# Kernel optimization log

Measured on AMD Instinct MI355X. Metric: run time of the kernel, lower is better.

The kernel has to match this reference:

```python
import jax, jax.numpy as jnp
import numpy as np

B = 131072
IN, H1, H2, OUT = 784, 128, 64, 10


def setup_inputs() -> dict:
    key = jax.random.key(0)
    ks = jax.random.split(key, 10)
    f16 = jnp.float16
    x = jax.random.normal(ks[0], (B, IN), dtype=f16)
    # int4 quantized weights: values in [-8, 7], stored as int32
    w1_q = jax.random.randint(ks[1], (H1, IN), -8, 8, dtype=jnp.int32)
    w2_q = jax.random.randint(ks[2], (H2, H1), -8, 8, dtype=jnp.int32)
    w3_q = jax.random.randint(ks[3], (OUT, H2), -8, 8, dtype=jnp.int32)
    # per-output-channel scales ~ kaiming-ish magnitude / 7 (int4 max)
    s1 = (jax.random.uniform(ks[4], (H1,), dtype=f16) * f16(0.02) + f16(0.005))
    s2 = (jax.random.uniform(ks[5], (H2,), dtype=f16) * f16(0.02) + f16(0.005))
    s3 = (jax.random.uniform(ks[6], (OUT,), dtype=f16) * f16(0.02) + f16(0.005))
    b1 = jax.random.normal(ks[7], (H1,), dtype=f16) * f16(0.01)
    b2 = jax.random.normal(ks[8], (H2,), dtype=f16) * f16(0.01)
    b3 = jax.random.normal(ks[9], (OUT,), dtype=f16) * f16(0.01)
    return {"x": x, "w1_q": w1_q, "s1": s1, "b1": b1,
            "w2_q": w2_q, "s2": s2, "b2": b2,
            "w3_q": w3_q, "s3": s3, "b3": b3}


def _qlinear(x, w_q, scale, bias):
    # W4A16: dequantize int4 weights with per-out-channel scale, fp16 GEMM + bias
    w = w_q.astype(jnp.float16) * scale[:, None]  # [out, in]
    return jnp.dot(x, w.T) + bias


def reference(x, w1_q, s1, b1, w2_q, s2, b2, w3_q, s3, b3):
    x = x.reshape(-1, IN)
    h = jax.nn.relu(_qlinear(x, w1_q, s1, b1))
    h = jax.nn.relu(_qlinear(h, w2_q, s2, b2))
    return _qlinear(h, w3_q, s3, b3)
```

## Files before the change

### kernel.cpp

```cpp
#include <hip/hip_runtime.h>
#include <hip/hip_bf16.h>

#define NROWS 131072
#define KIN   784
#define H1N   128
#define H2N   64
#define OUTN  10

#define W1P_DWORDS (25 * 4 * 128)
#define W2C_ELEMS  (16 * 64 * 8)
#define W3_ELEMS   (16 * 64)

typedef short s16x8 __attribute__((ext_vector_type(8)));
typedef float f32x4 __attribute__((ext_vector_type(4)));

typedef __hip_bfloat16 bf16;

static __device__ __forceinline__ short b2s(float f) {
    bf16 h = __float2bfloat16(f);
    return *reinterpret_cast<short*>(&h);
}

static __device__ __forceinline__ s16x8 cvt8(f32x4 a, f32x4 b) {
    s16x8 r;
    r[0] = b2s(a[0]); r[1] = b2s(a[1]); r[2] = b2s(a[2]); r[3] = b2s(a[3]);
    r[4] = b2s(b[0]); r[5] = b2s(b[1]); r[6] = b2s(b[2]); r[7] = b2s(b[3]);
    return r;
}

static __device__ __forceinline__ s16x8 unpack8(unsigned d) {
    s16x8 r;
#pragma unroll
    for (int j = 0; j < 8; ++j) {
        int v = ((int)(d << (28 - 4 * j))) >> 28;
        r[j] = b2s((float)v);
    }
    return r;
}

static __device__ __forceinline__ void gl2lds16(const void* g, char* l) {
    __builtin_amdgcn_global_load_lds(
        (const __attribute__((address_space(1))) void*)g,
        (__attribute__((address_space(3))) void*)l, 16, 0, 0);
}
static __device__ __forceinline__ void gl2lds4(const void* g, char* l) {
    __builtin_amdgcn_global_load_lds(
        (const __attribute__((address_space(1))) void*)g,
        (__attribute__((address_space(3))) void*)l, 4, 0, 0);
}

#define WAITV(N) do { asm volatile("s_waitcnt vmcnt(" #N ")" ::: "memory"); \
                      __builtin_amdgcn_sched_barrier(0); } while (0)
#define WAITL()  do { asm volatile("s_waitcnt lgkmcnt(0)" ::: "memory"); \
                      __builtin_amdgcn_sched_barrier(0); } while (0)
#define BAR()    __builtin_amdgcn_s_barrier()

__global__ __launch_bounds__(256) void dequant_kernel(
    const int* __restrict__ w1q, const float* __restrict__ s1,
    const int* __restrict__ w2q, const float* __restrict__ s2,
    const int* __restrict__ w3q, const float* __restrict__ s3,
    unsigned* __restrict__ w1p, bf16* __restrict__ w2c, bf16* __restrict__ w3d)
{
    const int total = W1P_DWORDS + W2C_ELEMS + W3_ELEMS;
    for (int i = blockIdx.x * blockDim.x + threadIdx.x; i < total;
         i += gridDim.x * blockDim.x) {
        if (i < W1P_DWORDS) {
            int kb = i >> 9, rem = i & 511;
            int kg = rem >> 7, col_s = rem & 127;
            int col = (col_s - 8 * kg) & 127;
            unsigned d = 0;
#pragma unroll
            for (int j = 0; j < 8; ++j) {
                int k = kb * 32 + kg * 8 + j;
                unsigned q = 0;
                if (k < KIN) q = (unsigned)w1q[col * KIN + k] & 0xFu;
                d |= q << (4 * j);
            }
            w1p[i] = d;
        } else if (i < W1P_DWORDS + W2C_ELEMS) {
            int t = i - W1P_DWORDS;
            int kb = t >> 9, rem = t & 511;
            int col = rem >> 3, j = rem & 7;
            int k = kb * 8 + j;
            w2c[t] = __float2bfloat16((float)w2q[col * H1N + k] * s2[col]);
        } else {
            int t = i - W1P_DWORDS - W2C_ELEMS;
            int r = t >> 6, c = t & 63;
            float v = 0.0f;
            if (r < OUTN) v = (float)w3q[r * H2N + c] * s3[r];
            w3d[t] = __float2bfloat16(v);
        }
    }
}

__global__ __launch_bounds__(256, 6) void mlp_kernel(
    const float* __restrict__ x,
    const unsigned* __restrict__ w1p,
    const bf16*  __restrict__ w2c,
    const bf16*  __restrict__ w3d,
    const float* __restrict__ s1,
    const float* __restrict__ b1,
    const float* __restrict__ b2,
    const float* __restrict__ b3,
    float* __restrict__ out)
{
    __shared__ __align__(16) char lds[20480];

    const int tid  = threadIdx.x;
    const int lane = tid & 63;
    const int wv   = tid >> 6;
    const int r16  = lane & 15;
    const int kg   = lane >> 4;
    const int kgo  = kg * 8;

    const int i3 = lane >> 3;
    const int i7 = lane & 7;
    const int sw = i7 ^ i3;
    const int adj = (sw >= 4) ? 16 : 0;

    const long long rowW = (long long)blockIdx.x * 64 + wv * 16;
    const float* gA = x + (rowW + i3) * (long long)KIN + sw * 4;
    const unsigned* gB = w1p + wv * 128 + lane;

    const int aoff0 = wv * 2048 + r16 * 128 + (((2 * kg) ^ (r16 & 7)) * 16);

#pragma unroll
    for (int w = 0; w < 2; ++w) {
        char* ad = lds + w * 8192 + wv * 2048;
        gl2lds16(gA + w * 32, ad);
        gl2lds16(gA + w * 32 + 8 * KIN, ad + 1024);
        char* bd = lds + 16384 + w * 2048 + wv * 512;
        const unsigned* gb = gB + w * 512;
        gl2lds4(gb, bd);
        gl2lds4(gb + 64, bd + 256);
    }

    f32x4 acc1[8];
#pragma unroll
    for (int j = 0; j < 8; ++j) acc1[j] = (f32x4){0.f, 0.f, 0.f, 0.f};

#pragma unroll 1
    for (int t = 0; t < 24; ++t) {
        WAITV(4);
        BAR();
        const char* sa = lds + (t & 1) * 8192;
        f32x4 q0 = *(const f32x4*)(sa + aoff0);
        f32x4 q1 = *(const f32x4*)(sa + (aoff0 ^ 16));
        const char* sbB = lds + 16384 + (t & 1) * 2048 + kg * 512;
        unsigned bd[8];
#pragma unroll
        for (int nj = 0; nj < 8; ++nj)
            bd[nj] = *(const unsigned*)(sbB + (((nj * 16 + r16 + 8 * kg) & 127) << 2));
        WAITL();
        BAR();
        if (t < 22) {
            char* ad = lds + (t & 1) * 8192 + wv * 2048;
            const float* g = gA + (t + 2) * 32;
            gl2lds16(g, ad);
            gl2lds16(g + 8 * KIN, ad + 1024);
            char* bdst = lds + 16384 + (t & 1) * 2048 + wv * 512;
            const unsigned* gb = gB + (t + 2) * 512;
            gl2lds4(gb, bdst);
            gl2lds4(gb + 64, bdst + 256);
        } else if (t == 22) {
            char* ad = lds + (t & 1) * 8192 + wv * 2048;
            const float* g = gA + 768 - adj;
            gl2lds16(g, ad);
            gl2lds16(g + 8 * KIN, ad + 1024);
            char* bdst = lds + 16384 + (t & 1) * 2048 + wv * 512;
            const unsigned* gb = gB + 24 * 512;
            gl2lds4(gb, bdst);
            gl2lds4(gb + 64, bdst + 256);
        }
        s16x8 a = cvt8(q0, q1);
#pragma unroll
        for (int nj = 0; nj < 8; ++nj) {
            s16x8 bf = unpack8(bd[nj]);
            acc1[nj] = __builtin_amdgcn_mfma_f32_16x16x32_bf16(a, bf, acc1[nj], 0, 0, 0);
        }
    }
    {
        WAITV(0);
        BAR();
        const char* sa = lds;
        f32x4 q0 = *(const f32x4*)(sa + aoff0);
        f32x4 q1 = *(const f32x4*)(sa + (aoff0 ^ 16));
        const char* sbB = lds + 16384 + kg * 512;
        unsigned bd[8];
#pragma unroll
        for (int nj = 0; nj < 8; ++nj)
            bd[nj] = *(const unsigned*)(sbB + (((nj * 16 + r16 + 8 * kg) & 127) << 2));
        WAITL();
        BAR();
        s16x8 a = cvt8(q0, q1);
#pragma unroll
        for (int nj = 0; nj < 8; ++nj) {
            s16x8 bf = unpack8(bd[nj]);
            acc1[nj] = __builtin_amdgcn_mfma_f32_16x16x32_bf16(a, bf, acc1[nj], 0, 0, 0);
        }
    }

    char* ar = lds + wv * 4224;
    short (*h1w)[132] = (short(*)[132])ar;
#pragma unroll
    for (int nj = 0; nj < 8; ++nj) {
        const int col = nj * 16 + r16;
        const float sc = s1[col];
        const float bb = b1[col];
#pragma unroll
        for (int r = 0; r < 4; ++r)
            h1w[kg * 4 + r][col] = b2s(fmaxf(acc1[nj][r] * sc + bb, 0.0f));
    }

    f32x4 acc2[4];
#pragma unroll
    for (int j = 0; j < 4; ++j) acc2[j] = (f32x4){0.f, 0.f, 0.f, 0.f};

#pragma unroll
    for (int it = 0; it < 4; ++it) {
        const int kk = it * 32 + kgo;
        s16x8 a = *(const s16x8*)&h1w[r16][kk];
        const bf16* bp2 = w2c + (size_t)(it * 4 + kg) * 512 + (size_t)r16 * 8;
#pragma unroll
        for (int nj = 0; nj < 4; ++nj) {
            s16x8 b = *(const s16x8*)(bp2 + nj * 128);
            acc2[nj] = __builtin_amdgcn_mfma_f32_16x16x32_bf16(a, b, acc2[nj], 0, 0, 0);
        }
    }

    short (*h2w)[68] = (short(*)[68])ar;
#pragma unroll
    for (int nj = 0; nj < 4; ++nj) {
        const int col = nj * 16 + r16;
        const float bb = b2[col];
#pragma unroll
        for (int r = 0; r < 4; ++r)
            h2w[kg * 4 + r][col] = b2s(fmaxf(acc2[nj][r] + bb, 0.0f));
    }

    f32x4 acc3 = (f32x4){0.f, 0.f, 0.f, 0.f};
#pragma unroll
    for (int it = 0; it < 2; ++it) {
        const int kk = it * 32 + kgo;
        s16x8 a = *(const s16x8*)&h2w[r16][kk];
        s16x8 b = *(const s16x8*)(w3d + r16 * H2N + kk);
        acc3 = __builtin_amdgcn_mfma_f32_16x16x32_bf16(a, b, acc3, 0, 0, 0);
    }

    float* ob = (float*)ar;
    const float bb3 = (r16 < OUTN) ? b3[r16] : 0.0f;
#pragma unroll
    for (int r = 0; r < 4; ++r) {
        const int row = kg * 4 + r;
        if (r16 < OUTN) ob[row * OUTN + r16] = acc3[r] + bb3;
    }
    const long long obase = rowW * OUTN;
    for (int i = lane; i < 16 * OUTN; i += 64) out[obase + i] = ob[i];
}

extern "C" void kernel_launch(void* const* d_in, const int* in_sizes, int n_in,
                              void* d_out, int out_size, void* d_ws, size_t ws_size,
                              hipStream_t stream) {
    const float* x   = (const float*)d_in[0];
    const int*   w1q = (const int*)d_in[1];
    const float* s1  = (const float*)d_in[2];
    const float* b1  = (const float*)d_in[3];
    const int*   w2q = (const int*)d_in[4];
    const float* s2  = (const float*)d_in[5];
    const float* b2  = (const float*)d_in[6];
    const int*   w3q = (const int*)d_in[7];
    const float* s3  = (const float*)d_in[8];
    const float* b3  = (const float*)d_in[9];
    float* out = (float*)d_out;

    unsigned* w1p = (unsigned*)d_ws;
    bf16* w2c = (bf16*)(w1p + W1P_DWORDS);
    bf16* w3d = w2c + W2C_ELEMS;

    dequant_kernel<<<128, 256, 0, stream>>>(w1q, s1, w2q, s2, w3q, s3, w1p, w2c, w3d);
    mlp_kernel<<<NROWS / 64, 256, 0, stream>>>(x, w1p, w2c, w3d, s1, b1, b2, b3, out);
}
```

Baseline: 117.7 us.

## Persistent blocks keep all int4 weights resident in LDS and stream row tiles

Moves from 2048 short blocks to 256 persistent 512-thread blocks. Each block loads every packed int4 weight (w2 and w3 now also int4 with scales applied in the epilogue) into about 112KB of dynamic LDS once, then streams 16-row x tiles through a double-buffered slot. Each wave owns 16 output columns of layer 1, and layers 2 and 3 run on a subset of waves per tile. This removes repeated per-block weight streaming and the bf16 w2/w3 global reads, at the cost of lower occupancy and extra barriers per tile.

```diff
diff --git a/kernel.cpp b/kernel.cpp
--- a/kernel.cpp
+++ b/kernel.cpp
@@ -7,27 +7,37 @@
 #define H2N   64
 #define OUTN  10
 
-#define W1P_DWORDS (25 * 4 * 128)
-#define W2C_ELEMS  (16 * 64 * 8)
-#define W3_ELEMS   (16 * 64)
+#define W1P_DW 12800
+#define W2P_DW 1024
+#define W3P_DW 128
+#define WTOT_DW (W1P_DW + W2P_DW + W3P_DW)
+
+#define OFF_W1P   0
+#define OFF_W2P   51200
+#define OFF_W3P   55296
+#define ROW_STR   1616
+#define SLOT_SZ   (16 * ROW_STR)
+#define OFF_SLOT0 55808
+#define OFF_SLOT1 (OFF_SLOT0 + SLOT_SZ)
+#define OFF_H1    107520
+#define OFF_H2    111872
+#define OFF_OB    114176
+#define LDS_BYTES 114816
 
 typedef short s16x8 __attribute__((ext_vector_type(8)));
 typedef float f32x4 __attribute__((ext_vector_type(4)));
-
 typedef __hip_bfloat16 bf16;
 
 static __device__ __forceinline__ short b2s(float f) {
     bf16 h = __float2bfloat16(f);
     return *reinterpret_cast<short*>(&h);
 }
-
 static __device__ __forceinline__ s16x8 cvt8(f32x4 a, f32x4 b) {
     s16x8 r;
     r[0] = b2s(a[0]); r[1] = b2s(a[1]); r[2] = b2s(a[2]); r[3] = b2s(a[3]);
     r[4] = b2s(b[0]); r[5] = b2s(b[1]); r[6] = b2s(b[2]); r[7] = b2s(b[3]);
     return r;
 }
-
 static __device__ __forceinline__ s16x8 unpack8(unsigned d) {
     s16x8 r;
 #pragma unroll
@@ -37,16 +47,10 @@
     }
     return r;
 }
-
 static __device__ __forceinline__ void gl2lds16(const void* g, char* l) {
     __builtin_amdgcn_global_load_lds(
         (const __attribute__((address_space(1))) void*)g,
         (__attribute__((address_space(3))) void*)l, 16, 0, 0);
-}
-static __device__ __forceinline__ void gl2lds4(const void* g, char* l) {
-    __builtin_amdgcn_global_load_lds(
-        (const __attribute__((address_space(1))) void*)g,
-        (__attribute__((address_space(3))) void*)l, 4, 0, 0);
 }
 
 #define WAITV(N) do { asm volatile("s_waitcnt vmcnt(" #N ")" ::: "memory"); \
@@ -56,19 +60,16 @@
 #define BAR()    __builtin_amdgcn_s_barrier()
 
 __global__ __launch_bounds__(256) void dequant_kernel(
-    const int* __restrict__ w1q, const float* __restrict__ s1,
-    const int* __restrict__ w2q, const float* __restrict__ s2,
-    const int* __restrict__ w3q, const float* __restrict__ s3,
-    unsigned* __restrict__ w1p, bf16* __restrict__ w2c, bf16* __restrict__ w3d)
+    const int* __restrict__ w1q, const int* __restrict__ w2q,
+    const int* __restrict__ w3q, unsigned* __restrict__ wpk)
 {
-    const int total = W1P_DWORDS + W2C_ELEMS + W3_ELEMS;
-    for (int i = blockIdx.x * blockDim.x + threadIdx.x; i < total;
+    for (int i = blockIdx.x * blockDim.x + threadIdx.x; i < WTOT_DW;
          i += gridDim.x * blockDim.x) {
-        if (i < W1P_DWORDS) {
+        unsigned d = 0;
+        if (i < W1P_DW) {
             int kb = i >> 9, rem = i & 511;
             int kg = rem >> 7, col_s = rem & 127;
             int col = (col_s - 8 * kg) & 127;
-            unsigned d = 0;
 #pragma unroll
             for (int j = 0; j < 8; ++j) {
                 int k = kb * 32 + kg * 8 + j;
@@ -76,186 +77,177 @@
                 if (k < KIN) q = (unsigned)w1q[col * KIN + k] & 0xFu;
                 d |= q << (4 * j);
             }
-            w1p[i] = d;
-        } else if (i < W1P_DWORDS + W2C_ELEMS) {
-            int t = i - W1P_DWORDS;
-            int kb = t >> 9, rem = t & 511;
-            int col = rem >> 3, j = rem & 7;
-            int k = kb * 8 + j;
-            w2c[t] = __float2bfloat16((float)w2q[col * H1N + k] * s2[col]);
+        } else if (i < W1P_DW + W2P_DW) {
+            int t = i - W1P_DW;
+            int kb = t >> 8, rem = t & 255;
+            int kg = rem >> 6, col = rem & 63;
+#pragma unroll
+            for (int j = 0; j < 8; ++j) {
+                int k = kb * 32 + kg * 8 + j;
+                d |= ((unsigned)w2q[col * H1N + k] & 0xFu) << (4 * j);
+            }
         } else {
-            int t = i - W1P_DWORDS - W2C_ELEMS;
-            int r = t >> 6, c = t & 63;
-            float v = 0.0f;
-            if (r < OUTN) v = (float)w3q[r * H2N + c] * s3[r];
-            w3d[t] = __float2bfloat16(v);
+            int t = i - W1P_DW - W2P_DW;
+            int kb = t >> 6, rem = t & 63;
+            int kg = rem >> 4, col = rem & 15;
+            if (col < OUTN) {
+#pragma unroll
+                for (int j = 0; j < 8; ++j) {
+                    int k = kb * 32 + kg * 8 + j;
+                    d |= ((unsigned)w3q[col * H2N + k] & 0xFu) << (4 * j);
+                }
+            }
         }
-    }
-}
-
-__global__ __launch_bounds__(256, 6) void mlp_kernel(
+        wpk[i] = d;
+    }
+}
+
+__global__ __launch_bounds__(512, 2) void mlp_kernel(
     const float* __restrict__ x,
-    const unsigned* __restrict__ w1p,
-    const bf16*  __restrict__ w2c,
-    const bf16*  __restrict__ w3d,
-    const float* __restrict__ s1,
-    const float* __restrict__ b1,
-    const float* __restrict__ b2,
-    const float* __restrict__ b3,
+    const unsigned* __restrict__ wpk,
+    const float* __restrict__ s1, const float* __restrict__ b1,
+    const float* __restrict__ s2, const float* __restrict__ b2,
+    const float* __restrict__ s3, const float* __restrict__ b3,
     float* __restrict__ out)
 {
-    __shared__ __align__(16) char lds[20480];
-
+    extern __shared__ __align__(16) char lds[];
     const int tid  = threadIdx.x;
     const int lane = tid & 63;
     const int wv   = tid >> 6;
     const int r16  = lane & 15;
     const int kg   = lane >> 4;
-    const int kgo  = kg * 8;
-
-    const int i3 = lane >> 3;
-    const int i7 = lane & 7;
-    const int sw = i7 ^ i3;
-    const int adj = (sw >= 4) ? 16 : 0;
-
-    const long long rowW = (long long)blockIdx.x * 64 + wv * 16;
-    const float* gA = x + (rowW + i3) * (long long)KIN + sw * 4;
-    const unsigned* gB = w1p + wv * 128 + lane;
-
-    const int aoff0 = wv * 2048 + r16 * 128 + (((2 * kg) ^ (r16 & 7)) * 16);
-
-#pragma unroll
-    for (int w = 0; w < 2; ++w) {
-        char* ad = lds + w * 8192 + wv * 2048;
-        gl2lds16(gA + w * 32, ad);
-        gl2lds16(gA + w * 32 + 8 * KIN, ad + 1024);
-        char* bd = lds + 16384 + w * 2048 + wv * 512;
-        const unsigned* gb = gB + w * 512;
-        gl2lds4(gb, bd);
-        gl2lds4(gb + 64, bd + 256);
-    }
-
-    f32x4 acc1[8];
-#pragma unroll
-    for (int j = 0; j < 8; ++j) acc1[j] = (f32x4){0.f, 0.f, 0.f, 0.f};
+
+    {
+        unsigned* lw = (unsigned*)lds;
+        for (int i = tid; i < WTOT_DW; i += 512) lw[i] = wpk[i];
+    }
+    const int col1 = wv * 16 + r16;
+    const float s1v = s1[col1], b1v = b1[col1];
+    const int col2 = (wv < 4) ? wv * 16 + r16 : 0;
+    const float s2v = s2[col2], b2v = b2[col2];
+    const int col3 = (r16 < OUTN) ? r16 : 0;
+    const float s3v = s3[col3], b3v = b3[col3];
+    __syncthreads();
+
+    const long long rowBlk = (long long)blockIdx.x * 512;
+    const int mlim0 = 32, mlim1 = 36;
+
+#define FETCH_HALF(H) do {                                                    \
+        const int t_ = (H) >> 1, p_ = (H) & 1;                                \
+        char* slot_ = lds + OFF_SLOT0 + ((H) & 1) * SLOT_SZ;                  \
+        const float* gr_ = x + (rowBlk + t_ * 16 + 2 * wv) * (long long)KIN;  \
+        const char* g_ = (const char*)gr_ + (p_ ? 1536 : 0);                  \
+        char* d_ = slot_ + (2 * wv) * ROW_STR;                                \
+        const int ml_ = p_ ? mlim1 : mlim0;                                   \
+        gl2lds16(g_ + lane * 16, d_);                                         \
+        if (lane < ml_) gl2lds16(g_ + 1024 + lane * 16, d_ + 1024);           \
+        const char* g2_ = g_ + KIN * 4;                                       \
+        char* d2_ = d_ + ROW_STR;                                             \
+        gl2lds16(g2_ + lane * 16, d2_);                                       \
+        if (lane < ml_) gl2lds16(g2_ + 1024 + lane * 16, d2_ + 1024);         \
+    } while (0)
+
+    FETCH_HALF(0);
+    FETCH_HALF(1);
+
+    f32x4 acc1 = (f32x4){0.f, 0.f, 0.f, 0.f};
 
 #pragma unroll 1
-    for (int t = 0; t < 24; ++t) {
-        WAITV(4);
+    for (int h = 0; h < 64; ++h) {
+        const int p = h & 1;
+        if (h == 63) { WAITV(0); } else { WAITV(4); }
         BAR();
-        const char* sa = lds + (t & 1) * 8192;
-        f32x4 q0 = *(const f32x4*)(sa + aoff0);
-        f32x4 q1 = *(const f32x4*)(sa + (aoff0 ^ 16));
-        const char* sbB = lds + 16384 + (t & 1) * 2048 + kg * 512;
-        unsigned bd[8];
-#pragma unroll
-        for (int nj = 0; nj < 8; ++nj)
-            bd[nj] = *(const unsigned*)(sbB + (((nj * 16 + r16 + 8 * kg) & 127) << 2));
+
+        const char* sl = lds + OFF_SLOT0 + (h & 1) * SLOT_SZ + r16 * ROW_STR;
+        if (p == 0) {
+            acc1 = (f32x4){0.f, 0.f, 0.f, 0.f};
+#pragma unroll
+            for (int w = 0; w < 12; ++w) {
+                f32x4 q0 = *(const f32x4*)(sl + w * 128 + kg * 32);
+                f32x4 q1 = *(const f32x4*)(sl + w * 128 + kg * 32 + 16);
+                unsigned bd = *(const unsigned*)(lds + OFF_W1P +
+                    ((w * 512) + kg * 128 + ((col1 + 8 * kg) & 127)) * 4);
+                acc1 = __builtin_amdgcn_mfma_f32_16x16x32_bf16(
+                    cvt8(q0, q1), unpack8(bd), acc1, 0, 0, 0);
+            }
+        } else {
+#pragma unroll
+            for (int w = 0; w < 12; ++w) {
+                f32x4 q0 = *(const f32x4*)(sl + w * 128 + kg * 32);
+                f32x4 q1 = *(const f32x4*)(sl + w * 128 + kg * 32 + 16);
+                unsigned bd = *(const unsigned*)(lds + OFF_W1P +
+                    (((w + 12) * 512) + kg * 128 + ((col1 + 8 * kg) & 127)) * 4);
+                acc1 = __builtin_amdgcn_mfma_f32_16x16x32_bf16(
+                    cvt8(q0, q1), unpack8(bd), acc1, 0, 0, 0);
+            }
+            {
+                f32x4 q0 = (f32x4){0.f,0.f,0.f,0.f}, q1 = q0;
+                if (kg < 2) {
+                    q0 = *(const f32x4*)(sl + 1536 + kg * 32);
+                    q1 = *(const f32x4*)(sl + 1536 + kg * 32 + 16);
+                }
+                unsigned bd = *(const unsigned*)(lds + OFF_W1P +
+                    ((24 * 512) + kg * 128 + ((col1 + 8 * kg) & 127)) * 4);
+                acc1 = __builtin_amdgcn_mfma_f32_16x16x32_bf16(
+                    cvt8(q0, q1), unpack8(bd), acc1, 0, 0, 0);
+            }
+#pragma unroll
+            for (int r = 0; r < 4; ++r) {
+                const int row = kg * 4 + r;
+                *(short*)(lds + OFF_H1 + row * 272 + col1 * 2) =
+                    b2s(fmaxf(acc1[r] * s1v + b1v, 0.0f));
+            }
+        }
+
         WAITL();
         BAR();
-        if (t < 22) {
-            char* ad = lds + (t & 1) * 8192 + wv * 2048;
-            const float* g = gA + (t + 2) * 32;
-            gl2lds16(g, ad);
-            gl2lds16(g + 8 * KIN, ad + 1024);
-            char* bdst = lds + 16384 + (t & 1) * 2048 + wv * 512;
-            const unsigned* gb = gB + (t + 2) * 512;
-            gl2lds4(gb, bdst);
-            gl2lds4(gb + 64, bdst + 256);
-        } else if (t == 22) {
-            char* ad = lds + (t & 1) * 8192 + wv * 2048;
-            const float* g = gA + 768 - adj;
-            gl2lds16(g, ad);
-            gl2lds16(g + 8 * KIN, ad + 1024);
-            char* bdst = lds + 16384 + (t & 1) * 2048 + wv * 512;
-            const unsigned* gb = gB + 24 * 512;
-            gl2lds4(gb, bdst);
-            gl2lds4(gb + 64, bdst + 256);
+
+        if (h + 2 < 64) FETCH_HALF(h + 2);
+
+        if (p) {
+            if (wv < 4) {
+                f32x4 acc2 = (f32x4){0.f, 0.f, 0.f, 0.f};
+#pragma unroll
+                for (int kb = 0; kb < 4; ++kb) {
+                    s16x8 a = *(const s16x8*)(lds + OFF_H1 + r16 * 272 +
+                                              (kb * 32 + kg * 8) * 2);
+                    unsigned bd = *(const unsigned*)(lds + OFF_W2P +
+                        (kb * 256 + kg * 64 + col2) * 4);
+                    acc2 = __builtin_amdgcn_mfma_f32_16x16x32_bf16(
+                        a, unpack8(bd), acc2, 0, 0, 0);
+                }
+#pragma unroll
+                for (int r = 0; r < 4; ++r) {
+                    const int row = kg * 4 + r;
+                    *(short*)(lds + OFF_H2 + row * 144 + col2 * 2) =
+                        b2s(fmaxf(acc2[r] * s2v + b2v, 0.0f));
+                }
+            }
+            WAITL();
+            BAR();
+            if (wv == 0) {
+                f32x4 acc3 = (f32x4){0.f, 0.f, 0.f, 0.f};
+#pragma unroll
+                for (int kb = 0; kb < 2; ++kb) {
+                    s16x8 a = *(const s16x8*)(lds + OFF_H2 + r16 * 144 +
+                                              (kb * 32 + kg * 8) * 2);
+                    unsigned bd = *(const unsigned*)(lds + OFF_W3P +
+                        (kb * 64 + kg * 16 + r16) * 4);
+                    acc3 = __builtin_amdgcn_mfma_f32_16x16x32_bf16(
+                        a, unpack8(bd), acc3, 0, 0, 0);
+                }
+                float* ob = (float*)(lds + OFF_OB);
+#pragma unroll
+                for (int r = 0; r < 4; ++r) {
+                    const int row = kg * 4 + r;
+                    if (r16 < OUTN) ob[row * OUTN + r16] = acc3[r] * s3v + b3v;
+                }
+                const long long obase = (rowBlk + (long long)(h >> 1) * 16) * OUTN;
+                for (int i = lane; i < 16 * OUTN; i += 64) out[obase + i] = ob[i];
+            }
         }
-        s16x8 a = cvt8(q0, q1);
-#pragma unroll
-        for (int nj = 0; nj < 8; ++nj) {
-            s16x8 bf = unpack8(bd[nj]);
-            acc1[nj] = __builtin_amdgcn_mfma_f32_16x16x32_bf16(a, bf, acc1[nj], 0, 0, 0);
-        }
-    }
-    {
-        WAITV(0);
-        BAR();
-        const char* sa = lds;
-        f32x4 q0 = *(const f32x4*)(sa + aoff0);
-        f32x4 q1 = *(const f32x4*)(sa + (aoff0 ^ 16));
-        const char* sbB = lds + 16384 + kg * 512;
-        unsigned bd[8];
-#pragma unroll
-        for (int nj = 0; nj < 8; ++nj)
-            bd[nj] = *(const unsigned*)(sbB + (((nj * 16 + r16 + 8 * kg) & 127) << 2));
-        WAITL();
-        BAR();
-        s16x8 a = cvt8(q0, q1);
-#pragma unroll
-        for (int nj = 0; nj < 8; ++nj) {
-            s16x8 bf = unpack8(bd[nj]);
-            acc1[nj] = __builtin_amdgcn_mfma_f32_16x16x32_bf16(a, bf, acc1[nj], 0, 0, 0);
-        }
-    }
-
-    char* ar = lds + wv * 4224;
-    short (*h1w)[132] = (short(*)[132])ar;
-#pragma unroll
-    for (int nj = 0; nj < 8; ++nj) {
-        const int col = nj * 16 + r16;
-        const float sc = s1[col];
-        const float bb = b1[col];
-#pragma unroll
-        for (int r = 0; r < 4; ++r)
-            h1w[kg * 4 + r][col] = b2s(fmaxf(acc1[nj][r] * sc + bb, 0.0f));
-    }
-
-    f32x4 acc2[4];
-#pragma unroll
-    for (int j = 0; j < 4; ++j) acc2[j] = (f32x4){0.f, 0.f, 0.f, 0.f};
-
-#pragma unroll
-    for (int it = 0; it < 4; ++it) {
-        const int kk = it * 32 + kgo;
-        s16x8 a = *(const s16x8*)&h1w[r16][kk];
-        const bf16* bp2 = w2c + (size_t)(it * 4 + kg) * 512 + (size_t)r16 * 8;
-#pragma unroll
-        for (int nj = 0; nj < 4; ++nj) {
-            s16x8 b = *(const s16x8*)(bp2 + nj * 128);
-            acc2[nj] = __builtin_amdgcn_mfma_f32_16x16x32_bf16(a, b, acc2[nj], 0, 0, 0);
-        }
-    }
-
-    short (*h2w)[68] = (short(*)[68])ar;
-#pragma unroll
-    for (int nj = 0; nj < 4; ++nj) {
-        const int col = nj * 16 + r16;
-        const float bb = b2[col];
-#pragma unroll
-        for (int r = 0; r < 4; ++r)
-            h2w[kg * 4 + r][col] = b2s(fmaxf(acc2[nj][r] + bb, 0.0f));
-    }
-
-    f32x4 acc3 = (f32x4){0.f, 0.f, 0.f, 0.f};
-#pragma unroll
-    for (int it = 0; it < 2; ++it) {
-        const int kk = it * 32 + kgo;
-        s16x8 a = *(const s16x8*)&h2w[r16][kk];
-        s16x8 b = *(const s16x8*)(w3d + r16 * H2N + kk);
-        acc3 = __builtin_amdgcn_mfma_f32_16x16x32_bf16(a, b, acc3, 0, 0, 0);
-    }
-
-    float* ob = (float*)ar;
-    const float bb3 = (r16 < OUTN) ? b3[r16] : 0.0f;
-#pragma unroll
-    for (int r = 0; r < 4; ++r) {
-        const int row = kg * 4 + r;
-        if (r16 < OUTN) ob[row * OUTN + r16] = acc3[r] + bb3;
-    }
-    const long long obase = rowW * OUTN;
-    for (int i = lane; i < 16 * OUTN; i += 64) out[obase + i] = ob[i];
+    }
+#undef FETCH_HALF
 }
 
 extern "C" void kernel_launch(void* const* d_in, const int* in_sizes, int n_in,
@@ -273,10 +265,15 @@
     const float* b3  = (const float*)d_in[9];
     float* out = (float*)d_out;
 
-    unsigned* w1p = (unsigned*)d_ws;
-    bf16* w2c = (bf16*)(w1p + W1P_DWORDS);
-    bf16* w3d = w2c + W2C_ELEMS;
-
-    dequant_kernel<<<128, 256, 0, stream>>>(w1q, s1, w2q, s2, w3q, s3, w1p, w2c, w3d);
-    mlp_kernel<<<NROWS / 64, 256, 0, stream>>>(x, w1p, w2c, w3d, s1, b1, b2, b3, out);
-}
+    unsigned* wpk = (unsigned*)d_ws;
+
+    static int attr_set = 0;
+    if (!attr_set) {
+        hipFuncSetAttribute((const void*)mlp_kernel,
+                            hipFuncAttributeMaxDynamicSharedMemorySize, LDS_BYTES);
+        attr_set = 1;
+    }
+
+    dequant_kernel<<<64, 256, 0, stream>>>(w1q, w2q, w3q, wpk);
+    mlp_kernel<<<256, 512, LDS_BYTES, stream>>>(x, wpk, s1, b1, s2, b2, s3, b3, out);
+}
```

Result: slower. 183.9 us (+56.3%).

## Tile layer-1 GEMM as 2x2 wave grid sharing int4 unpack

Applied to the files above, without the earlier changes.

Layer 1 is re-partitioned so each of the four waves computes a 32-row by 64-column tile instead of 16 rows by all 128 columns. Each unpacked int4 weight fragment now feeds two MFMAs, which halves the per-wave int4-to-bf16 unpack work at the cost of a second fp32-to-bf16 conversion for activations. Because each wave now produces only part of every h1 row, h1 is written to a block-shared LDS buffer and a block barrier is added before layer 2. LDS grows to 25600 bytes and the launch-bounds occupancy hint drops from 6 to 5.

```diff
diff --git a/kernel.cpp b/kernel.cpp
--- a/kernel.cpp
+++ b/kernel.cpp
@@ -7,27 +7,24 @@
 #define H2N   64
 #define OUTN  10
 
-#define W1P_DWORDS (25 * 4 * 128)
-#define W2C_ELEMS  (16 * 64 * 8)
-#define W3_ELEMS   (16 * 64)
+#define W1P_DW    12800
+#define W2C_ELEMS (16 * 64 * 8)
+#define W3_ELEMS  (16 * 64)
 
 typedef short s16x8 __attribute__((ext_vector_type(8)));
 typedef float f32x4 __attribute__((ext_vector_type(4)));
-
 typedef __hip_bfloat16 bf16;
 
 static __device__ __forceinline__ short b2s(float f) {
     bf16 h = __float2bfloat16(f);
     return *reinterpret_cast<short*>(&h);
 }
-
 static __device__ __forceinline__ s16x8 cvt8(f32x4 a, f32x4 b) {
     s16x8 r;
     r[0] = b2s(a[0]); r[1] = b2s(a[1]); r[2] = b2s(a[2]); r[3] = b2s(a[3]);
     r[4] = b2s(b[0]); r[5] = b2s(b[1]); r[6] = b2s(b[2]); r[7] = b2s(b[3]);
     return r;
 }
-
 static __device__ __forceinline__ s16x8 unpack8(unsigned d) {
     s16x8 r;
 #pragma unroll
@@ -37,7 +34,6 @@
     }
     return r;
 }
-
 static __device__ __forceinline__ void gl2lds16(const void* g, char* l) {
     __builtin_amdgcn_global_load_lds(
         (const __attribute__((address_space(1))) void*)g,
@@ -61,10 +57,10 @@
     const int* __restrict__ w3q, const float* __restrict__ s3,
     unsigned* __restrict__ w1p, bf16* __restrict__ w2c, bf16* __restrict__ w3d)
 {
-    const int total = W1P_DWORDS + W2C_ELEMS + W3_ELEMS;
+    const int total = W1P_DW + W2C_ELEMS + W3_ELEMS;
     for (int i = blockIdx.x * blockDim.x + threadIdx.x; i < total;
          i += gridDim.x * blockDim.x) {
-        if (i < W1P_DWORDS) {
+        if (i < W1P_DW) {
             int kb = i >> 9, rem = i & 511;
             int kg = rem >> 7, col_s = rem & 127;
             int col = (col_s - 8 * kg) & 127;
@@ -77,14 +73,14 @@
                 d |= q << (4 * j);
             }
             w1p[i] = d;
-        } else if (i < W1P_DWORDS + W2C_ELEMS) {
-            int t = i - W1P_DWORDS;
+        } else if (i < W1P_DW + W2C_ELEMS) {
+            int t = i - W1P_DW;
             int kb = t >> 9, rem = t & 511;
             int col = rem >> 3, j = rem & 7;
             int k = kb * 8 + j;
             w2c[t] = __float2bfloat16((float)w2q[col * H1N + k] * s2[col]);
         } else {
-            int t = i - W1P_DWORDS - W2C_ELEMS;
+            int t = i - W1P_DW - W2C_ELEMS;
             int r = t >> 6, c = t & 63;
             float v = 0.0f;
             if (r < OUTN) v = (float)w3q[r * H2N + c] * s3[r];
@@ -93,7 +89,7 @@
     }
 }
 
-__global__ __launch_bounds__(256, 6) void mlp_kernel(
+__global__ __launch_bounds__(256, 5) void mlp_kernel(
     const float* __restrict__ x,
     const unsigned* __restrict__ w1p,
     const bf16*  __restrict__ w2c,
@@ -104,7 +100,7 @@
     const float* __restrict__ b3,
     float* __restrict__ out)
 {
-    __shared__ __align__(16) char lds[20480];
+    __shared__ __align__(16) char lds[25600];
 
     const int tid  = threadIdx.x;
     const int lane = tid & 63;
@@ -112,105 +108,119 @@
     const int r16  = lane & 15;
     const int kg   = lane >> 4;
     const int kgo  = kg * 8;
+    const int rg   = wv >> 1;
+    const int cg   = wv & 1;
 
     const int i3 = lane >> 3;
     const int i7 = lane & 7;
     const int sw = i7 ^ i3;
     const int adj = (sw >= 4) ? 16 : 0;
 
-    const long long rowW = (long long)blockIdx.x * 64 + wv * 16;
-    const float* gA = x + (rowW + i3) * (long long)KIN + sw * 4;
-    const unsigned* gB = w1p + wv * 128 + lane;
-
-    const int aoff0 = wv * 2048 + r16 * 128 + (((2 * kg) ^ (r16 & 7)) * 16);
+    const long long rowBlk = (long long)blockIdx.x * 64;
+    const float* gA0 = x + (rowBlk + wv * 16 + i3) * (long long)KIN + sw * 4;
+    const float* gA1 = gA0 + 8LL * KIN;
+    const unsigned* gBp = w1p + wv * 128 + lane;
+
+    const int aoff = (rg * 32 + r16) * 128 + (((2 * kg) ^ (r16 & 7)) * 16);
+    const int bcol = cg * 64 + r16 + 8 * kg;
 
 #pragma unroll
     for (int w = 0; w < 2; ++w) {
         char* ad = lds + w * 8192 + wv * 2048;
-        gl2lds16(gA + w * 32, ad);
-        gl2lds16(gA + w * 32 + 8 * KIN, ad + 1024);
+        gl2lds16(gA0 + w * 32, ad);
+        gl2lds16(gA1 + w * 32, ad + 1024);
         char* bd = lds + 16384 + w * 2048 + wv * 512;
-        const unsigned* gb = gB + w * 512;
-        gl2lds4(gb, bd);
-        gl2lds4(gb + 64, bd + 256);
-    }
-
-    f32x4 acc1[8];
-#pragma unroll
-    for (int j = 0; j < 8; ++j) acc1[j] = (f32x4){0.f, 0.f, 0.f, 0.f};
+        gl2lds4(gBp + w * 512, bd);
+        gl2lds4(gBp + w * 512 + 64, bd + 256);
+    }
+
+    f32x4 acc1[2][4];
+#pragma unroll
+    for (int i = 0; i < 2; ++i)
+#pragma unroll
+        for (int j = 0; j < 4; ++j) acc1[i][j] = (f32x4){0.f, 0.f, 0.f, 0.f};
 
 #pragma unroll 1
     for (int t = 0; t < 24; ++t) {
         WAITV(4);
         BAR();
         const char* sa = lds + (t & 1) * 8192;
-        f32x4 q0 = *(const f32x4*)(sa + aoff0);
-        f32x4 q1 = *(const f32x4*)(sa + (aoff0 ^ 16));
-        const char* sbB = lds + 16384 + (t & 1) * 2048 + kg * 512;
-        unsigned bd[8];
-#pragma unroll
-        for (int nj = 0; nj < 8; ++nj)
-            bd[nj] = *(const unsigned*)(sbB + (((nj * 16 + r16 + 8 * kg) & 127) << 2));
+        f32x4 q00 = *(const f32x4*)(sa + aoff);
+        f32x4 q01 = *(const f32x4*)(sa + (aoff ^ 16));
+        f32x4 q10 = *(const f32x4*)(sa + aoff + 2048);
+        f32x4 q11 = *(const f32x4*)(sa + (aoff ^ 16) + 2048);
+        const char* sb = lds + 16384 + (t & 1) * 2048 + kg * 512;
+        unsigned bw4[4];
+#pragma unroll
+        for (int nj = 0; nj < 4; ++nj)
+            bw4[nj] = *(const unsigned*)(sb + (((bcol + nj * 16) & 127) << 2));
         WAITL();
         BAR();
-        if (t < 22) {
+        {
+            const int w = t + 2;
             char* ad = lds + (t & 1) * 8192 + wv * 2048;
-            const float* g = gA + (t + 2) * 32;
-            gl2lds16(g, ad);
-            gl2lds16(g + 8 * KIN, ad + 1024);
-            char* bdst = lds + 16384 + (t & 1) * 2048 + wv * 512;
-            const unsigned* gb = gB + (t + 2) * 512;
-            gl2lds4(gb, bdst);
-            gl2lds4(gb + 64, bdst + 256);
-        } else if (t == 22) {
-            char* ad = lds + (t & 1) * 8192 + wv * 2048;
-            const float* g = gA + 768 - adj;
-            gl2lds16(g, ad);
-            gl2lds16(g + 8 * KIN, ad + 1024);
-            char* bdst = lds + 16384 + (t & 1) * 2048 + wv * 512;
-            const unsigned* gb = gB + 24 * 512;
-            gl2lds4(gb, bdst);
-            gl2lds4(gb + 64, bdst + 256);
-        }
-        s16x8 a = cvt8(q0, q1);
-#pragma unroll
-        for (int nj = 0; nj < 8; ++nj) {
-            s16x8 bf = unpack8(bd[nj]);
-            acc1[nj] = __builtin_amdgcn_mfma_f32_16x16x32_bf16(a, bf, acc1[nj], 0, 0, 0);
+            char* bd = lds + 16384 + (t & 1) * 2048 + wv * 512;
+            if (w < 24) {
+                gl2lds16(gA0 + w * 32, ad);
+                gl2lds16(gA1 + w * 32, ad + 1024);
+                gl2lds4(gBp + w * 512, bd);
+                gl2lds4(gBp + w * 512 + 64, bd + 256);
+            } else if (w == 24) {
+                gl2lds16(gA0 + 768 - adj, ad);
+                gl2lds16(gA1 + 768 - adj, ad + 1024);
+                gl2lds4(gBp + 24 * 512, bd);
+                gl2lds4(gBp + 24 * 512 + 64, bd + 256);
+            }
+        }
+        s16x8 a0 = cvt8(q00, q01);
+        s16x8 a1 = cvt8(q10, q11);
+#pragma unroll
+        for (int nj = 0; nj < 4; ++nj) {
+            s16x8 bf = unpack8(bw4[nj]);
+            acc1[0][nj] = __builtin_amdgcn_mfma_f32_16x16x32_bf16(a0, bf, acc1[0][nj], 0, 0, 0);
+            acc1[1][nj] = __builtin_amdgcn_mfma_f32_16x16x32_bf16(a1, bf, acc1[1][nj], 0, 0, 0);
         }
     }
     {
         WAITV(0);
         BAR();
         const char* sa = lds;
-        f32x4 q0 = *(const f32x4*)(sa + aoff0);
-        f32x4 q1 = *(const f32x4*)(sa + (aoff0 ^ 16));
-        const char* sbB = lds + 16384 + kg * 512;
-        unsigned bd[8];
-#pragma unroll
-        for (int nj = 0; nj < 8; ++nj)
-            bd[nj] = *(const unsigned*)(sbB + (((nj * 16 + r16 + 8 * kg) & 127) << 2));
+        f32x4 q00 = *(const f32x4*)(sa + aoff);
+        f32x4 q01 = *(const f32x4*)(sa + (aoff ^ 16));
+        f32x4 q10 = *(const f32x4*)(sa + aoff + 2048);
+        f32x4 q11 = *(const f32x4*)(sa + (aoff ^ 16) + 2048);
+        const char* sb = lds + 16384 + kg * 512;
+        unsigned bw4[4];
+#pragma unroll
+        for (int nj = 0; nj < 4; ++nj)
+            bw4[nj] = *(const unsigned*)(sb + (((bcol + nj * 16) & 127) << 2));
         WAITL();
         BAR();
-        s16x8 a = cvt8(q0, q1);
-#pragma unroll
-        for (int nj = 0; nj < 8; ++nj) {
-            s16x8 bf = unpack8(bd[nj]);
-            acc1[nj] = __builtin_amdgcn_mfma_f32_16x16x32_bf16(a, bf, acc1[nj], 0, 0, 0);
-        }
-    }
-
-    char* ar = lds + wv * 4224;
-    short (*h1w)[132] = (short(*)[132])ar;
-#pragma unroll
-    for (int nj = 0; nj < 8; ++nj) {
-        const int col = nj * 16 + r16;
+        s16x8 a0 = cvt8(q00, q01);
+        s16x8 a1 = cvt8(q10, q11);
+#pragma unroll
+        for (int nj = 0; nj < 4; ++nj) {
+            s16x8 bf = unpack8(bw4[nj]);
+            acc1[0][nj] = __builtin_amdgcn_mfma_f32_16x16x32_bf16(a0, bf, acc1[0][nj], 0, 0, 0);
+            acc1[1][nj] = __builtin_amdgcn_mfma_f32_16x16x32_bf16(a1, bf, acc1[1][nj], 0, 0, 0);
+        }
+    }
+
+    short* h1s = (short*)lds;
+#pragma unroll
+    for (int nj = 0; nj < 4; ++nj) {
+        const int col = cg * 64 + nj * 16 + r16;
         const float sc = s1[col];
         const float bb = b1[col];
 #pragma unroll
-        for (int r = 0; r < 4; ++r)
-            h1w[kg * 4 + r][col] = b2s(fmaxf(acc1[nj][r] * sc + bb, 0.0f));
-    }
+        for (int mi = 0; mi < 2; ++mi)
+#pragma unroll
+            for (int r = 0; r < 4; ++r) {
+                const int row = rg * 32 + mi * 16 + kg * 4 + r;
+                h1s[row * 132 + col] = b2s(fmaxf(acc1[mi][nj][r] * sc + bb, 0.0f));
+            }
+    }
+    __syncthreads();
 
     f32x4 acc2[4];
 #pragma unroll
@@ -219,7 +229,7 @@
 #pragma unroll
     for (int it = 0; it < 4; ++it) {
         const int kk = it * 32 + kgo;
-        s16x8 a = *(const s16x8*)&h1w[r16][kk];
+        s16x8 a = *(const s16x8*)(h1s + (wv * 16 + r16) * 132 + kk);
         const bf16* bp2 = w2c + (size_t)(it * 4 + kg) * 512 + (size_t)r16 * 8;
 #pragma unroll
         for (int nj = 0; nj < 4; ++nj) {
@@ -228,33 +238,33 @@
         }
     }
 
-    short (*h2w)[68] = (short(*)[68])ar;
+    short* h2s = (short*)(lds + 16896);
 #pragma unroll
     for (int nj = 0; nj < 4; ++nj) {
         const int col = nj * 16 + r16;
         const float bb = b2[col];
 #pragma unroll
         for (int r = 0; r < 4; ++r)
-            h2w[kg * 4 + r][col] = b2s(fmaxf(acc2[nj][r] + bb, 0.0f));
+            h2s[(wv * 16 + kg * 4 + r) * 68 + col] = b2s(fmaxf(acc2[nj][r] + bb, 0.0f));
     }
 
     f32x4 acc3 = (f32x4){0.f, 0.f, 0.f, 0.f};
 #pragma unroll
     for (int it = 0; it < 2; ++it) {
         const int kk = it * 32 + kgo;
-        s16x8 a = *(const s16x8*)&h2w[r16][kk];
+        s16x8 a = *(const s16x8*)(h2s + (wv * 16 + r16) * 68 + kk);
         s16x8 b = *(const s16x8*)(w3d + r16 * H2N + kk);
         acc3 = __builtin_amdgcn_mfma_f32_16x16x32_bf16(a, b, acc3, 0, 0, 0);
     }
 
-    float* ob = (float*)ar;
+    float* ob = (float*)(lds + (wv * 16) * 264);
     const float bb3 = (r16 < OUTN) ? b3[r16] : 0.0f;
 #pragma unroll
     for (int r = 0; r < 4; ++r) {
         const int row = kg * 4 + r;
         if (r16 < OUTN) ob[row * OUTN + r16] = acc3[r] + bb3;
     }
-    const long long obase = rowW * OUTN;
+    const long long obase = (rowBlk + wv * 16) * OUTN;
     for (int i = lane; i < 16 * OUTN; i += 64) out[obase + i] = ob[i];
 }
 
@@ -274,7 +284,7 @@
     float* out = (float*)d_out;
 
     unsigned* w1p = (unsigned*)d_ws;
-    bf16* w2c = (bf16*)(w1p + W1P_DWORDS);
+    bf16* w2c = (bf16*)(w1p + W1P_DW);
     bf16* w3d = w2c + W2C_ELEMS;
 
     dequant_kernel<<<128, 256, 0, stream>>>(w1q, s1, w2q, s2, w3q, s3, w1p, w2c, w3d);
```

New measurement: 95.54 us. -18.8%, faster.
